# Kernel tuning notes

Hardware: AMD Instinct MI355X
Metric: run time of the kernel (lower is better)

Reference implementation:

```python
import jax, jax.numpy as jnp
import numpy as np
import math

HIDDEN = 2048
HEADS = 16
G = 4          # kv groups (= self.num_group after the module's head_num//num_group)
HPG = HEADS // G  # q heads per group
D = HIDDEN // HEADS  # 128


def setup_inputs() -> dict:
    key = jax.random.key(0)
    ks = jax.random.split(key, 9)
    B, S = 2, 2048
    s = 0.02
    return {
        "x": jax.random.normal(ks[0], (B, S, HIDDEN), dtype=jnp.float32),
        "Wq": jax.random.normal(ks[1], (HIDDEN, HIDDEN), dtype=jnp.float32) * s,
        "bq": jnp.zeros((HIDDEN,), jnp.float32),
        "Wk": jax.random.normal(ks[2], (HIDDEN, G * D), dtype=jnp.float32) * s,
        "bk": jnp.zeros((G * D,), jnp.float32),
        "Wv": jax.random.normal(ks[3], (HIDDEN, G * D), dtype=jnp.float32) * s,
        "bv": jnp.zeros((G * D,), jnp.float32),
        "Wo": jax.random.normal(ks[4], (HIDDEN, HIDDEN), dtype=jnp.float32) * s,
        "bo": jnpp if False else jnp.zeros((HIDDEN,), jnp.float32),
    }


def reference(x, Wq, bq, Wk, bk, Wv, bv, Wo, bo):
    B, S, H = x.shape
    # projections (torch Linear with W stored as (in, out))
    q = (x @ Wq + bq).reshape(B, S, G, HPG, D)   # (B,S,G,Hpg,D)
    k = (x @ Wk + bk).reshape(B, S, G, D)        # (B,S,G,D)
    v = (x @ Wv + bv).reshape(B, S, G, D)
    scale = 1.0 / math.sqrt(D)
    # scores: each of the Hpg query heads in a group shares the group's K/V
    scores = jnp.einsum("bsghd,btgd->bghst", q, k) * scale  # (B,G,Hpg,S,S)
    attn = jax.nn.softmax(scores, axis=-1)
    # dropout is identity in eval mode
    o = jnp.einsum("bghst,btgd->bsghd", attn, v).reshape(B, S, H)
    return o @ Wo + bo
```

## Files before the change

kernel.cpp:

```cpp
#include <hip/hip_runtime.h>

#define HID   2048
#define KD    2048
#define GQ    4
#define HPGQ  4
#define DH    128
#define SEQ   2048
#define NBATCH 2
#define NTOK  (NBATCH * SEQ)
#define NQKV  3072

typedef unsigned short u16;
typedef unsigned int   u32;
using bf16x8 = __attribute__((ext_vector_type(8))) __bf16;
using bf16x2 = __attribute__((ext_vector_type(2))) __bf16;
using f32x4  = __attribute__((ext_vector_type(4))) float;
using u32x4  = __attribute__((ext_vector_type(4))) u32;

#if __has_builtin(__builtin_amdgcn_exp2f)
#define FEXP2(x) __builtin_amdgcn_exp2f(x)
#else
#define FEXP2(x) exp2f(x)
#endif

#define QSCALE 0.12751744f

__device__ __forceinline__ u16 f2bf(float f) {
  union { float f; u32 u; } v; v.f = f;
  u32 u = v.u + 0x7fffu + ((v.u >> 16) & 1u);
  return (u16)(u >> 16);
}

__device__ __forceinline__ u32 pk2(float a, float b) {
  bf16x2 t;
  t[0] = (__bf16)a;
  t[1] = (__bf16)b;
  return __builtin_bit_cast(u32, t);
}

__device__ __forceinline__ void gl16(const void* g, void* l) {
  __builtin_amdgcn_global_load_lds((const __attribute__((address_space(1))) u32*)g,
                                   (__attribute__((address_space(3))) u32*)l, 16, 0, 0);
}

__device__ __forceinline__ int swz(int r, int c) {
  return (c & ~7) | ((c ^ r ^ (r >> 3)) & 7);
}

__global__ __launch_bounds__(256) void k_cvt_bf16(const float* __restrict__ in,
                                                  u16* __restrict__ out, int n4) {
  int i = blockIdx.x * 256 + threadIdx.x;
  if (i < n4) {
    const float4 v = ((const float4*)in)[i];
    ushort4 o;
    o.x = f2bf(v.x); o.y = f2bf(v.y); o.z = f2bf(v.z); o.w = f2bf(v.w);
    ((ushort4*)out)[i] = o;
  }
}

__global__ __launch_bounds__(256) void k_trans_cvt(const float* __restrict__ W,
                                                   u16* __restrict__ WT,
                                                   int K, int N, int rowoff) {
  __shared__ float tile[32][33];
  const int tx = threadIdx.x, ty = threadIdx.y;
  const int k0 = blockIdx.y * 32, n0 = blockIdx.x * 32;
#pragma unroll
  for (int i = 0; i < 4; ++i)
    tile[ty + 8 * i][tx] = W[(size_t)(k0 + ty + 8 * i) * N + (n0 + tx)];
  __syncthreads();
#pragma unroll
  for (int i = 0; i < 4; ++i)
    WT[(size_t)(rowoff + n0 + ty + 8 * i) * K + (k0 + tx)] = f2bf(tile[tx][ty + 8 * i]);
}


#define STG256(OP, ROWB, KTB, LB)                                                  \
  { _Pragma("unroll") for (int i = 0; i < 2; ++i)                                  \
      gl16((OP) + (size_t)(ROWB) * KD + (KTB) + stOffE[i],                         \
           S + (LB) + (i * 512 + t) * 8); }

#define STAGE_TILE(D, KTB)                                                         \
  STG256(A,  m0,       (KTB), (D) * 32768 + 0);                                    \
  STG256(A,  m0 + 128, (KTB), (D) * 32768 + 8192);                                 \
  STG256(Bt, n0,       (KTB), (D) * 32768 + 16384);                                \
  STG256(Bt, n0 + 128, (KTB), (D) * 32768 + 24576);

#define RDA(D, M, KC) (*(const bf16x8*)((const char*)S + (D) * 65536 + (M) * 2048 + (aQ ^ ((KC) << 6))))
#define RDB(D, N, KC) (*(const bf16x8*)((const char*)S + (D) * 65536 + (N) * 2048 + (bQ ^ ((KC) << 6))))

#define MFMA16(MB, NB)                                                             \
  __builtin_amdgcn_s_setprio(1);                                                   \
  _Pragma("unroll") for (int m = 0; m < 4; ++m)                                    \
    _Pragma("unroll") for (int n = 0; n < 2; ++n)                                  \
      _Pragma("unroll") for (int kc = 0; kc < 2; ++kc)                             \
        acc[(MB) + m][(NB) + n] = __builtin_amdgcn_mfma_f32_16x16x32_bf16(         \
            afr[m][kc], bfr[(NB) + n][kc], acc[(MB) + m][(NB) + n], 0, 0, 0);      \
  __builtin_amdgcn_s_setprio(0);

#define ITER256(D, KTN, PRE)                                                       \
  do {                                                                             \
                                     \
    _Pragma("unroll") for (int m = 0; m < 4; ++m)                                  \
      _Pragma("unroll") for (int kc = 0; kc < 2; ++kc)                             \
        afr[m][kc] = RDA(D, m, kc);                                                \
    _Pragma("unroll") for (int n = 0; n < 2; ++n)                                  \
      _Pragma("unroll") for (int kc = 0; kc < 2; ++kc)                             \
        bfr[n][kc] = RDB(D, n, kc);                                                \
    __builtin_amdgcn_s_barrier();                                                  \
    MFMA16(0, 0)                                                                   \
    __builtin_amdgcn_s_barrier();                                                  \
                                             \
    _Pragma("unroll") for (int n = 2; n < 4; ++n)                                  \
      _Pragma("unroll") for (int kc = 0; kc < 2; ++kc)                             \
        bfr[n][kc] = RDB(D, n, kc);                                                \
    __builtin_amdgcn_s_barrier();                                                  \
    MFMA16(0, 2)                                                                   \
    __builtin_amdgcn_s_barrier();                                                  \
                                 \
    _Pragma("unroll") for (int m = 0; m < 4; ++m)                                  \
      _Pragma("unroll") for (int kc = 0; kc < 2; ++kc)                             \
        afr[m][kc] = RDA(D, 4 + m, kc);                                            \
    __builtin_amdgcn_s_barrier();                                                  \
    MFMA16(4, 2)                                                                   \
    __builtin_amdgcn_s_barrier();                                                  \
             \
    if (PRE) {                                                                     \
      STAGE_TILE(D, KTN);                                                          \
      asm volatile("s_waitcnt vmcnt(8)" ::: "memory");                             \
    } else {                                                                       \
      asm volatile("s_waitcnt vmcnt(0)" ::: "memory");                             \
    }                                                                              \
    __builtin_amdgcn_s_barrier();                                                  \
    MFMA16(4, 0)                                                                   \
    __builtin_amdgcn_s_barrier();                                                  \
  } while (0)

__global__ __launch_bounds__(512, 1) void k_gemm_qkv(
    const u16* __restrict__ A, const u16* __restrict__ Bt,
    u16* __restrict__ qkv, u16* __restrict__ vT,
    const float* __restrict__ bq, const float* __restrict__ bk,
    const float* __restrict__ bv) {
  __shared__ u16 S[65536];
  const int t = threadIdx.x, l = t & 63, w = t >> 6;
  const int lr = l & 15, lk = l >> 4;
  const int wm = w >> 2, wn = w & 3;
  const int m0 = blockIdx.y * 256, n0 = blockIdx.x * 256;

  int stOffE[2];
#pragma unroll
  for (int i = 0; i < 2; ++i) {
    const int e = i * 512 + t;
    const int r = e >> 3;
    stOffE[i] = r * KD + ((e & 7) ^ (r & 7)) * 8;
  }
  const int qb = lr * 128 + (((lr >> 2) & 1) << 6) + ((lk ^ (lr & 3)) << 4);
  const int aQ = wm * 16384 + qb;
  const int bQ = 32768 + (wn >> 1) * 16384 + (wn & 1) * 8192 + qb;

  f32x4 acc[8][4] = {};
  bf16x8 afr[4][2], bfr[4][2];

  STAGE_TILE(0, 0);
  STAGE_TILE(1, 64);
  asm volatile("s_waitcnt vmcnt(8)" ::: "memory");
  __builtin_amdgcn_s_barrier();

  for (int j = 0; j < 28; j += 2) {
    ITER256(0, (j + 2) * 64, true);
    ITER256(1, (j + 3) * 64, true);
  }
  ITER256(0, 30 * 64, true);
  ITER256(1, 31 * 64, true);
  ITER256(0, 0, false);
  ITER256(1, 0, false);

  const int gmB = m0 + wm * 128, gnB = n0 + wn * 64;
#pragma unroll
  for (int m = 0; m < 8; ++m) {
    const int row0 = gmB + m * 16 + lk * 4;
#pragma unroll
    for (int n = 0; n < 4; ++n) {
      const int col = gnB + n * 16 + lr;
      float bias, qs = 1.0f;
      if (col < HID) { bias = bq[col]; qs = QSCALE; }
      else if (col < HID + 512) bias = bk[col - HID];
      else bias = bv[col - HID - 512];
      if (col < HID + 512) {
#pragma unroll
        for (int r = 0; r < 4; ++r)
          qkv[(size_t)(row0 + r) * NQKV + col] = f2bf((acc[m][n][r] + bias) * qs);
      } else {
        const int gg = (col - 2560) >> 7, d = (col - 2560) & 127;
        const int b = row0 >> 11, s0 = row0 & 2047;
        ushort4 pk;
        pk.x = f2bf(acc[m][n][0] + bias);
        pk.y = f2bf(acc[m][n][1] + bias);
        pk.z = f2bf(acc[m][n][2] + bias);
        pk.w = f2bf(acc[m][n][3] + bias);
        *(ushort4*)(vT + ((size_t)(b * GQ + gg) * DH + d) * SEQ + s0) = pk;
      }
    }
  }
}

#define GEMM_STEP(CUR, NXT, K0N, PRE)                                              \
  do {                                                                             \
    if (PRE) {                                                                     \
      const u16* aB = A  + (size_t)m0 * KD + (K0N);                                \
      const u16* bB = Bt + (size_t)n0 * KD + (K0N);                                \
      _Pragma("unroll")                                                            \
      for (int i = 0; i < 2; ++i) {                                                \
        gl16(aB + stOff[i], S + (NXT)*4096 + (i * 256 + t) * 8);                   \
        gl16(bB + stOff[i], S + 8192 + (NXT)*4096 + (i * 256 + t) * 8);            \
      }                                                                            \
      asm volatile("s_waitcnt vmcnt(4)" ::: "memory");                             \
    } else {                                                                       \
      asm volatile("s_waitcnt vmcnt(0)" ::: "memory");                             \
    }                                                                              \
    __builtin_amdgcn_s_barrier();                                                  \
    bf16x8 af[4], bfr[4];                                                          \
    _Pragma("unroll")                                                              \
    for (int m = 0; m < 4; ++m)                                                    \
      af[m] = *(const bf16x8*)((const char*)S + (CUR)*8192 + m * 1024 + aAddr);    \
    _Pragma("unroll")                                                              \
    for (int n = 0; n < 4; ++n)                                                    \
      bfr[n] = *(const bf16x8*)((const char*)S + 16384 + (CUR)*8192 + n * 1024 + bAddr); \
    __builtin_amdgcn_s_setprio(1);                                                 \
    _Pragma("unroll")                                                              \
    for (int m = 0; m < 4; ++m)                                                    \
      _Pragma("unroll")                                                            \
      for (int n = 0; n < 4; ++n)                                                  \
        acc[m][n] = __builtin_amdgcn_mfma_f32_16x16x32_bf16(af[m], bfr[n], acc[m][n], 0, 0, 0); \
    __builtin_amdgcn_s_setprio(0);                                                 \
    __builtin_amdgcn_s_barrier();                                                  \
  } while (0)

__global__ __launch_bounds__(256) void k_gemm_o(
    const u16* __restrict__ A, const u16* __restrict__ Bt,
    const float* __restrict__ bo, float* __restrict__ C) {
  __shared__ u16 S[16384];
  const int t = threadIdx.x, l = t & 63, w = t >> 6;
  const int lr = l & 15, lk = l >> 4;
  const int wr = w >> 1, wc = w & 1;
  const int m0 = blockIdx.y * 128, n0 = blockIdx.x * 128;
  int stOff[2];
#pragma unroll
  for (int i = 0; i < 2; ++i) {
    const int e = i * 256 + t;
    const int r = e >> 2;
    const int cs = (e & 3) ^ ((r >> 1) & 3);
    stOff[i] = r * KD + cs * 8;
  }
  const int axor = (lk ^ ((lr >> 1) & 3)) << 4;
  const int aAddr = (wr * 64 + lr) * 64 + axor;
  const int bAddr = (wc * 64 + lr) * 64 + axor;
  f32x4 acc[4][4] = {};
  {
    const u16* aB = A  + (size_t)m0 * KD;
    const u16* bB = Bt + (size_t)n0 * KD;
#pragma unroll
    for (int i = 0; i < 2; ++i) {
      gl16(aB + stOff[i], S + (i * 256 + t) * 8);
      gl16(bB + stOff[i], S + 8192 + (i * 256 + t) * 8);
    }
  }
  for (int kt = 0; kt < KD / 32 - 2; kt += 2) {
    GEMM_STEP(0, 1, (kt + 1) * 32, true);
    GEMM_STEP(1, 0, (kt + 2) * 32, true);
  }
  GEMM_STEP(0, 1, (KD / 32 - 1) * 32, true);
  GEMM_STEP(1, 0, 0, false);

  const int gm = m0 + wr * 64, gn = n0 + wc * 64;
#pragma unroll
  for (int m = 0; m < 4; ++m) {
    const int row0 = gm + m * 16 + lk * 4;
#pragma unroll
    for (int n = 0; n < 4; ++n) {
      const int col = gn + n * 16 + lr;
      const float bias = bo[col];
#pragma unroll
      for (int r = 0; r < 4; ++r)
        C[(size_t)(row0 + r) * HID + col] = acc[m][n][r] + bias;
    }
  }
}

#define ATTN_ITER(KS, VS, KN, VN, TTV, PRE)                                        \
  do {                                                                             \
    if (PRE) {                                                                     \
      const int t0n = ((start + (TTV) + 1) & (NT - 1)) * 32;                       \
      const u16* kbT = kbase + (size_t)t0n * NQKV;                                 \
      const u16* vbT = vbase + t0n;                                                \
      _Pragma("unroll")                                                            \
      for (int i = 0; i < 2; ++i) {                                                \
        gl16(kbT + kOffE[i], (KN) + (i * 256 + t) * 8);                            \
        gl16(vbT + vOffE[i], (VN) + (i * 256 + t) * 8);                            \
      }                                                                            \
      asm volatile("s_waitcnt vmcnt(4)" ::: "memory");                             \
    } else {                                                                       \
      asm volatile("s_waitcnt vmcnt(0)" ::: "memory");                             \
    }                                                                              \
    __builtin_amdgcn_s_barrier();                                                  \
    f32x4 sc[2][2] = {};                                                           \
    __builtin_amdgcn_s_setprio(1);                                                 \
    _Pragma("unroll")                                                              \
    for (int kk = 0; kk < 4; ++kk) {                                               \
      bf16x8 kf[2];                                                                \
      _Pragma("unroll")                                                            \
      for (int mk = 0; mk < 2; ++mk) {                                             \
        const int LIT = (mk << 12) ^ ((kk >> 1) << 7) ^ ((kk & 1) << 6) ^ (mk << 5); \
        kf[mk] = *(const bf16x8*)((const char*)(KS) + (kQ0 ^ LIT));                \
      }                                                                            \
      _Pragma("unroll")                                                            \
      for (int nq = 0; nq < 2; ++nq)                                               \
        _Pragma("unroll")                                                          \
        for (int mk = 0; mk < 2; ++mk)                                             \
          sc[nq][mk] = __builtin_amdgcn_mfma_f32_16x16x32_bf16(kf[mk], qf[nq][kk], sc[nq][mk], 0, 0, 0); \
    }                                                                              \
    __builtin_amdgcn_s_setprio(0);                                                 \
    bf16x8 pa[2];                                                                  \
    _Pragma("unroll")                                                              \
    for (int nq = 0; nq < 2; ++nq) {                                               \
      u32 w0 = pk2(FEXP2(sc[nq][0][0]), FEXP2(sc[nq][0][1]));                      \
      u32 w1 = pk2(FEXP2(sc[nq][0][2]), FEXP2(sc[nq][0][3]));                      \
      u32 w2 = pk2(FEXP2(sc[nq][1][0]), FEXP2(sc[nq][1][1]));                      \
      u32 w3 = pk2(FEXP2(sc[nq][1][2]), FEXP2(sc[nq][1][3]));                      \
      asm("v_permlane32_swap_b32 %0, %1" : "+v"(w0), "+v"(w2));                    \
      asm("v_permlane32_swap_b32 %0, %1" : "+v"(w1), "+v"(w3));                    \
      asm("v_permlane16_swap_b32 %0, %1" : "+v"(w0), "+v"(w2));                    \
      asm("v_permlane16_swap_b32 %0, %1" : "+v"(w1), "+v"(w3));                    \
      u32x4 u = {w0, w1, w2, w3};                                                  \
      pa[nq] = __builtin_bit_cast(bf16x8, u);                                      \
    }                                                                              \
    __builtin_amdgcn_s_setprio(1);                                                 \
    _Pragma("unroll")                                                              \
    for (int nq = 0; nq < 2; ++nq)                                                 \
      acc_s[nq] = __builtin_amdgcn_mfma_f32_16x16x32_bf16(pa[nq], vones, acc_s[nq], 0, 0, 0); \
    _Pragma("unroll")                                                              \
    for (int nd = 0; nd < 8; ++nd) {                                               \
      const bf16x8 vf = *(const bf16x8*)((const char*)(VS) + vQ0 + nd * 1024);     \
      _Pragma("unroll")                                                            \
      for (int nq = 0; nq < 2; ++nq)                                               \
        acc_o[nq][nd] = __builtin_amdgcn_mfma_f32_16x16x32_bf16(pa[nq], vf, acc_o[nq][nd], 0, 0, 0); \
    }                                                                              \
    __builtin_amdgcn_s_setprio(0);                                                 \
    __builtin_amdgcn_s_barrier();                                                  \
  } while (0)

__global__ __launch_bounds__(256, 2) void k_attn(
    const u16* __restrict__ qkv, const u16* __restrict__ vT, u16* __restrict__ o_ws) {
  __shared__ u16 smem[16384];
  u16* const kb0 = smem;
  u16* const kb1 = smem + 4096;
  u16* const vb0 = smem + 8192;
  u16* const vb1 = smem + 12288;

  const int t = threadIdx.x, l = t & 63, w = t >> 6;
  const int lr = l & 15, lk = l >> 4;
  const int f = blockIdx.x;
  const int bg = f & 7;
  const int h = (f >> 3) & 3;
  const int qt = f >> 5;
  const int b = bg >> 2, g = bg & 3;
  const int q0 = qt * 128;
  const int qcol = (g * HPGQ + h) * DH;
  const u16* qbase = qkv + (size_t)(b * SEQ) * NQKV;
  const u16* kbase = qbase + HID + g * DH;
  const u16* vbase = vT + (size_t)(b * GQ + g) * DH * SEQ;

  const int NT = SEQ / 32;
  const int start = (qt * 5 + h * 9) & (NT - 1);

  const int kQ0 = lr * 256 + ((lk ^ (lr & 7) ^ (lr >> 3)) << 4);
  const int vQ0 = lr * 64 + ((lk ^ ((lr >> 1) & 3)) << 4);
  int kOffE[2], vOffE[2];
#pragma unroll
  for (int i = 0; i < 2; ++i) {
    const int e = i * 256 + t;
    const int r = e >> 4, c = e & 15;
    kOffE[i] = r * NQKV + swz(r, c) * 8;
    const int rv = e >> 2, cv = e & 3;
    vOffE[i] = rv * SEQ + ((cv ^ ((rv >> 1) & 3)) * 8);
  }

  bf16x8 qf[2][4];
#pragma unroll
  for (int nq = 0; nq < 2; ++nq)
#pragma unroll
    for (int kk = 0; kk < 4; ++kk)
      qf[nq][kk] = *(const bf16x8*)(qbase + (size_t)(q0 + w * 32 + nq * 16 + lr) * NQKV +
                                    qcol + kk * 32 + lk * 8);

  {
    const int t00 = start * 32;
    const u16* kbT = kbase + (size_t)t00 * NQKV;
    const u16* vbT = vbase + t00;
#pragma unroll
    for (int i = 0; i < 2; ++i) {
      gl16(kbT + kOffE[i], kb0 + (i * 256 + t) * 8);
      gl16(vbT + vOffE[i], vb0 + (i * 256 + t) * 8);
    }
  }

  f32x4 acc_o[2][8] = {};
  f32x4 acc_s[2] = {};

  bf16x8 vones;
#pragma unroll
  for (int j = 0; j < 8; ++j) vones[j] = (lr == 0) ? (__bf16)1.0f : (__bf16)0.0f;

  for (int tp = 0; tp < NT - 2; tp += 2) {
    ATTN_ITER(kb0, vb0, kb1, vb1, tp, true);
    ATTN_ITER(kb1, vb1, kb0, vb0, tp + 1, true);
  }
  ATTN_ITER(kb0, vb0, kb1, vb1, NT - 2, true);
  ATTN_ITER(kb1, vb1, kb0, vb0, NT - 1, false);

#pragma unroll
  for (int nq = 0; nq < 2; ++nq)
#pragma unroll
    for (int r = 0; r < 4; ++r) {
      const float s = __shfl(acc_s[nq][r], l & 48);
      const float inv = 1.0f / s;
      const int q = q0 + w * 32 + nq * 16 + lk * 4 + r;
#pragma unroll
      for (int nd = 0; nd < 8; ++nd) {
        const int d = nd * 16 + lr;
        o_ws[(size_t)(b * SEQ + q) * HID + qcol + d] = f2bf(acc_o[nq][nd][r] * inv);
      }
    }
}

extern "C" void kernel_launch(void* const* d_in, const int* in_sizes, int n_in,
                              void* d_out, int out_size, void* d_ws, size_t ws_size,
                              hipStream_t stream) {
  const float* x  = (const float*)d_in[0];
  const float* Wq = (const float*)d_in[1];
  const float* bq = (const float*)d_in[2];
  const float* Wk = (const float*)d_in[3];
  const float* bk = (const float*)d_in[4];
  const float* Wv = (const float*)d_in[5];
  const float* bv = (const float*)d_in[6];
  const float* Wo = (const float*)d_in[7];
  const float* bo = (const float*)d_in[8];
  float* out = (float*)d_out;

  char* ws = (char*)d_ws;
  u16* x_bf  = (u16*)ws;  ws += (size_t)NTOK * KD * 2;
  u16* qkvT  = (u16*)ws;  ws += (size_t)NQKV * KD * 2;
  u16* WoT   = (u16*)ws;  ws += (size_t)HID * KD * 2;
  u16* qkv   = (u16*)ws;  ws += (size_t)NTOK * NQKV * 2;
  u16* vTb   = (u16*)ws;  ws += (size_t)NBATCH * GQ * DH * SEQ * 2;
  u16* o_ws  = x_bf;

  k_cvt_bf16<<<(NTOK * KD / 4 + 255) / 256, 256, 0, stream>>>(x, x_bf, NTOK * KD / 4);
  k_trans_cvt<<<dim3(HID / 32, KD / 32), dim3(32, 8), 0, stream>>>(Wq, qkvT, KD, HID, 0);
  k_trans_cvt<<<dim3(512 / 32, KD / 32), dim3(32, 8), 0, stream>>>(Wk, qkvT, KD, 512, 2048);
  k_trans_cvt<<<dim3(512 / 32, KD / 32), dim3(32, 8), 0, stream>>>(Wv, qkvT, KD, 512, 2560);
  k_trans_cvt<<<dim3(HID / 32, KD / 32), dim3(32, 8), 0, stream>>>(Wo, WoT, KD, HID, 0);

  k_gemm_qkv<<<dim3(NQKV / 256, NTOK / 256), 512, 0, stream>>>(x_bf, qkvT, qkv, vTb, bq, bk, bv);
  k_attn<<<SEQ / 128 * NBATCH * GQ * HPGQ, 256, 0, stream>>>(qkv, vTb, o_ws);
  k_gemm_o<<<dim3(HID / 128, NTOK / 128), 256, 0, stream>>>(o_ws, WoT, bo, out);
}
```

Before: 206.5 us.

## Retile QKV GEMM to 256x192 for full CU coverage and merge transpose launches

Changes the QKV projection GEMM tile from 256x256 to 256x192 so the grid has 256 blocks, matching the CU count and avoiding a partial second wave. It restructures LDS staging into separate A and B loads with adjusted waitcnts and a three-column-tile inner schedule. It also merges the four weight transpose/convert launches into one 3D-grid kernel to cut launch overhead. The smaller N tile lowers per-block arithmetic intensity and slightly increases A re-reads.

```diff
diff --git a/kernel.cpp b/kernel.cpp
--- a/kernel.cpp
+++ b/kernel.cpp
@@ -58,80 +58,101 @@
   }
 }
 
-__global__ __launch_bounds__(256) void k_trans_cvt(const float* __restrict__ W,
-                                                   u16* __restrict__ WT,
-                                                   int K, int N, int rowoff) {
+__global__ __launch_bounds__(256) void k_trans_all(
+    const float* __restrict__ Wq, const float* __restrict__ Wk,
+    const float* __restrict__ Wv, const float* __restrict__ Wo,
+    u16* __restrict__ qkvT, u16* __restrict__ WoT) {
   __shared__ float tile[32][33];
+  const int z = blockIdx.z;
+  const float* W = (z == 0) ? Wq : (z == 1) ? Wk : (z == 2) ? Wv : Wo;
+  u16* WT = (z == 3) ? WoT : qkvT;
+  const int N = (z == 1 || z == 2) ? 512 : 2048;
+  const int rowoff = (z == 1) ? 2048 : (z == 2) ? 2560 : 0;
+  const int n0 = blockIdx.x * 32;
+  if (n0 >= N) return;
   const int tx = threadIdx.x, ty = threadIdx.y;
-  const int k0 = blockIdx.y * 32, n0 = blockIdx.x * 32;
+  const int k0 = blockIdx.y * 32;
 #pragma unroll
   for (int i = 0; i < 4; ++i)
     tile[ty + 8 * i][tx] = W[(size_t)(k0 + ty + 8 * i) * N + (n0 + tx)];
   __syncthreads();
 #pragma unroll
   for (int i = 0; i < 4; ++i)
-    WT[(size_t)(rowoff + n0 + ty + 8 * i) * K + (k0 + tx)] = f2bf(tile[tx][ty + 8 * i]);
-}
-
-
-#define STG256(OP, ROWB, KTB, LB)                                                  \
+    WT[(size_t)(rowoff + n0 + ty + 8 * i) * KD + (k0 + tx)] = f2bf(tile[tx][ty + 8 * i]);
+}
+
+
+#define QBUF 114688
+#define BUFB 57344
+
+#define STG128(OP, ROWB, KTB, LBYTE)                                               \
   { _Pragma("unroll") for (int i = 0; i < 2; ++i)                                  \
       gl16((OP) + (size_t)(ROWB) * KD + (KTB) + stOffE[i],                         \
-           S + (LB) + (i * 512 + t) * 8); }
-
-#define STAGE_TILE(D, KTB)                                                         \
-  STG256(A,  m0,       (KTB), (D) * 32768 + 0);                                    \
-  STG256(A,  m0 + 128, (KTB), (D) * 32768 + 8192);                                 \
-  STG256(Bt, n0,       (KTB), (D) * 32768 + 16384);                                \
-  STG256(Bt, n0 + 128, (KTB), (D) * 32768 + 24576);
-
-#define RDA(D, M, KC) (*(const bf16x8*)((const char*)S + (D) * 65536 + (M) * 2048 + (aQ ^ ((KC) << 6))))
-#define RDB(D, N, KC) (*(const bf16x8*)((const char*)S + (D) * 65536 + (N) * 2048 + (bQ ^ ((KC) << 6))))
-
-#define MFMA16(MB, NB)                                                             \
-  __builtin_amdgcn_s_setprio(1);                                                   \
+           (u16*)((char*)S + (LBYTE)) + (i * 512 + t) * 8); }
+#define STG64(OP, ROWB, KTB, LBYTE)                                                \
+  gl16((OP) + (size_t)(ROWB) * KD + (KTB) + stOffE[0],                             \
+       (u16*)((char*)S + (LBYTE)) + t * 8);
+
+#define STAGE_B(D, KTB)                                                            \
+  STG128(Bt, n0b,       (KTB), (D) * BUFB + 32768);                                \
+  STG64 (Bt, n0b + 128, (KTB), (D) * BUFB + 49152);
+#define STAGE_A(D, KTB)                                                            \
+  STG128(A,  m0,        (KTB), (D) * BUFB + 0);                                    \
+  STG128(A,  m0 + 128,  (KTB), (D) * BUFB + 16384);
+
+#define RDA(D, M, KC) (*(const bf16x8*)((const char*)S + (D) * BUFB + (M) * 2048 + (aQ ^ ((KC) << 6))))
+#define RDB(D, NT, KC) (*(const bf16x8*)((const char*)S + (D) * BUFB + (NT) * 2048 + (bQ ^ ((KC) << 6))))
+
+#define MFMA8(MB, NT)                                                              \
   _Pragma("unroll") for (int m = 0; m < 4; ++m)                                    \
-    _Pragma("unroll") for (int n = 0; n < 2; ++n)                                  \
-      _Pragma("unroll") for (int kc = 0; kc < 2; ++kc)                             \
-        acc[(MB) + m][(NB) + n] = __builtin_amdgcn_mfma_f32_16x16x32_bf16(         \
-            afr[m][kc], bfr[(NB) + n][kc], acc[(MB) + m][(NB) + n], 0, 0, 0);      \
-  __builtin_amdgcn_s_setprio(0);
-
-#define ITER256(D, KTN, PRE)                                                       \
+    _Pragma("unroll") for (int kc = 0; kc < 2; ++kc)                               \
+      acc[(MB) + m][NT] = __builtin_amdgcn_mfma_f32_16x16x32_bf16(                 \
+          afr[m][kc], bfr[NT][kc], acc[(MB) + m][NT], 0, 0, 0);
+
+#define ITERQ(D, KTN, PRE)                                                         \
   do {                                                                             \
-                                     \
+                                                                           \
     _Pragma("unroll") for (int m = 0; m < 4; ++m)                                  \
       _Pragma("unroll") for (int kc = 0; kc < 2; ++kc)                             \
         afr[m][kc] = RDA(D, m, kc);                                                \
-    _Pragma("unroll") for (int n = 0; n < 2; ++n)                                  \
+    _Pragma("unroll") for (int nt = 0; nt < 2; ++nt)                               \
       _Pragma("unroll") for (int kc = 0; kc < 2; ++kc)                             \
-        bfr[n][kc] = RDB(D, n, kc);                                                \
-    __builtin_amdgcn_s_barrier();                                                  \
-    MFMA16(0, 0)                                                                   \
-    __builtin_amdgcn_s_barrier();                                                  \
-                                             \
-    _Pragma("unroll") for (int n = 2; n < 4; ++n)                                  \
-      _Pragma("unroll") for (int kc = 0; kc < 2; ++kc)                             \
-        bfr[n][kc] = RDB(D, n, kc);                                                \
-    __builtin_amdgcn_s_barrier();                                                  \
-    MFMA16(0, 2)                                                                   \
-    __builtin_amdgcn_s_barrier();                                                  \
-                                 \
+        bfr[nt][kc] = RDB(D, nt, kc);                                              \
+    asm volatile("s_waitcnt lgkmcnt(8)" ::: "memory");                             \
+    __builtin_amdgcn_s_barrier();                                                  \
+    __builtin_amdgcn_s_setprio(1);                                                 \
+    MFMA8(0, 0) MFMA8(0, 1)                                                        \
+    __builtin_amdgcn_s_setprio(0);                                                 \
+    __builtin_amdgcn_s_barrier();                                                  \
+                                                                           \
+    _Pragma("unroll") for (int kc = 0; kc < 2; ++kc)                               \
+      bfr[2][kc] = RDB(D, 2, kc);                                                  \
+    __builtin_amdgcn_s_barrier();                                                  \
+    __builtin_amdgcn_s_setprio(1);                                                 \
+    MFMA8(0, 2)                                                                    \
+    __builtin_amdgcn_s_setprio(0);                                                 \
+    __builtin_amdgcn_s_barrier();                                                  \
+                                                                           \
     _Pragma("unroll") for (int m = 0; m < 4; ++m)                                  \
       _Pragma("unroll") for (int kc = 0; kc < 2; ++kc)                             \
         afr[m][kc] = RDA(D, 4 + m, kc);                                            \
-    __builtin_amdgcn_s_barrier();                                                  \
-    MFMA16(4, 2)                                                                   \
-    __builtin_amdgcn_s_barrier();                                                  \
-             \
+    if (PRE) { STAGE_B(D, KTN); }                                                  \
+    __builtin_amdgcn_s_barrier();                                                  \
+    __builtin_amdgcn_s_setprio(1);                                                 \
+    MFMA8(4, 2)                                                                    \
+    __builtin_amdgcn_s_setprio(0);                                                 \
+    __builtin_amdgcn_s_barrier();                                                  \
+                                                                           \
     if (PRE) {                                                                     \
-      STAGE_TILE(D, KTN);                                                          \
-      asm volatile("s_waitcnt vmcnt(8)" ::: "memory");                             \
+      STAGE_A(D, KTN);                                                             \
+      asm volatile("s_waitcnt vmcnt(7)" ::: "memory");                             \
     } else {                                                                       \
       asm volatile("s_waitcnt vmcnt(0)" ::: "memory");                             \
     }                                                                              \
     __builtin_amdgcn_s_barrier();                                                  \
-    MFMA16(4, 0)                                                                   \
+    __builtin_amdgcn_s_setprio(1);                                                 \
+    MFMA8(4, 0) MFMA8(4, 1)                                                        \
+    __builtin_amdgcn_s_setprio(0);                                                 \
     __builtin_amdgcn_s_barrier();                                                  \
   } while (0)
 
@@ -140,11 +161,11 @@
     u16* __restrict__ qkv, u16* __restrict__ vT,
     const float* __restrict__ bq, const float* __restrict__ bk,
     const float* __restrict__ bv) {
-  __shared__ u16 S[65536];
+  __shared__ u16 S[QBUF / 2];
   const int t = threadIdx.x, l = t & 63, w = t >> 6;
   const int lr = l & 15, lk = l >> 4;
   const int wm = w >> 2, wn = w & 3;
-  const int m0 = blockIdx.y * 256, n0 = blockIdx.x * 256;
+  const int m0 = blockIdx.y * 256, n0b = blockIdx.x * 192;
 
   int stOffE[2];
 #pragma unroll
@@ -155,32 +176,30 @@
   }
   const int qb = lr * 128 + (((lr >> 2) & 1) << 6) + ((lk ^ (lr & 3)) << 4);
   const int aQ = wm * 16384 + qb;
-  const int bQ = 32768 + (wn >> 1) * 16384 + (wn & 1) * 8192 + qb;
-
-  f32x4 acc[8][4] = {};
-  bf16x8 afr[4][2], bfr[4][2];
-
-  STAGE_TILE(0, 0);
-  STAGE_TILE(1, 64);
-  asm volatile("s_waitcnt vmcnt(8)" ::: "memory");
+  const int bQ = 32768 + wn * 6144 + qb;
+
+  f32x4 acc[8][3] = {};
+  bf16x8 afr[4][2], bfr[3][2];
+
+  STAGE_A(0, 0);  STAGE_B(0, 0);
+  STAGE_A(1, 64); STAGE_B(1, 64);
+  asm volatile("s_waitcnt vmcnt(7)" ::: "memory");
   __builtin_amdgcn_s_barrier();
 
-  for (int j = 0; j < 28; j += 2) {
-    ITER256(0, (j + 2) * 64, true);
-    ITER256(1, (j + 3) * 64, true);
-  }
-  ITER256(0, 30 * 64, true);
-  ITER256(1, 31 * 64, true);
-  ITER256(0, 0, false);
-  ITER256(1, 0, false);
-
-  const int gmB = m0 + wm * 128, gnB = n0 + wn * 64;
+  for (int j = 0; j < 30; j += 2) {
+    ITERQ(0, (j + 2) * 64, true);
+    ITERQ(1, (j + 3) * 64, true);
+  }
+  ITERQ(0, 0, false);
+  ITERQ(1, 0, false);
+
+  const int gmB = m0 + wm * 128, gnB = n0b + wn * 48;
 #pragma unroll
   for (int m = 0; m < 8; ++m) {
     const int row0 = gmB + m * 16 + lk * 4;
 #pragma unroll
-    for (int n = 0; n < 4; ++n) {
-      const int col = gnB + n * 16 + lr;
+    for (int nt = 0; nt < 3; ++nt) {
+      const int col = gnB + nt * 16 + lr;
       float bias, qs = 1.0f;
       if (col < HID) { bias = bq[col]; qs = QSCALE; }
       else if (col < HID + 512) bias = bk[col - HID];
@@ -188,15 +207,15 @@
       if (col < HID + 512) {
 #pragma unroll
         for (int r = 0; r < 4; ++r)
-          qkv[(size_t)(row0 + r) * NQKV + col] = f2bf((acc[m][n][r] + bias) * qs);
+          qkv[(size_t)(row0 + r) * NQKV + col] = f2bf((acc[m][nt][r] + bias) * qs);
       } else {
         const int gg = (col - 2560) >> 7, d = (col - 2560) & 127;
         const int b = row0 >> 11, s0 = row0 & 2047;
         ushort4 pk;
-        pk.x = f2bf(acc[m][n][0] + bias);
-        pk.y = f2bf(acc[m][n][1] + bias);
-        pk.z = f2bf(acc[m][n][2] + bias);
-        pk.w = f2bf(acc[m][n][3] + bias);
+        pk.x = f2bf(acc[m][nt][0] + bias);
+        pk.y = f2bf(acc[m][nt][1] + bias);
+        pk.z = f2bf(acc[m][nt][2] + bias);
+        pk.w = f2bf(acc[m][nt][3] + bias);
         *(ushort4*)(vT + ((size_t)(b * GQ + gg) * DH + d) * SEQ + s0) = pk;
       }
     }
@@ -210,8 +229,8 @@
       const u16* bB = Bt + (size_t)n0 * KD + (K0N);                                \
       _Pragma("unroll")                                                            \
       for (int i = 0; i < 2; ++i) {                                                \
-        gl16(aB + stOff[i], S + (NXT)*4096 + (i * 256 + t) * 8);                   \
-        gl16(bB + stOff[i], S + 8192 + (NXT)*4096 + (i * 256 + t) * 8);            \
+        gl16(aB + stOff[i], So + (NXT)*4096 + (i * 256 + t) * 8);                  \
+        gl16(bB + stOff[i], So + 8192 + (NXT)*4096 + (i * 256 + t) * 8);           \
       }                                                                            \
       asm volatile("s_waitcnt vmcnt(4)" ::: "memory");                             \
     } else {                                                                       \
@@ -221,10 +240,10 @@
     bf16x8 af[4], bfr[4];                                                          \
     _Pragma("unroll")                                                              \
     for (int m = 0; m < 4; ++m)                                                    \
-      af[m] = *(const bf16x8*)((const char*)S + (CUR)*8192 + m * 1024 + aAddr);    \
+      af[m] = *(const bf16x8*)((const char*)So + (CUR)*8192 + m * 1024 + aAddr);   \
     _Pragma("unroll")                                                              \
     for (int n = 0; n < 4; ++n)                                                    \
-      bfr[n] = *(const bf16x8*)((const char*)S + 16384 + (CUR)*8192 + n * 1024 + bAddr); \
+      bfr[n] = *(const bf16x8*)((const char*)So + 16384 + (CUR)*8192 + n * 1024 + bAddr); \
     __builtin_amdgcn_s_setprio(1);                                                 \
     _Pragma("unroll")                                                              \
     for (int m = 0; m < 4; ++m)                                                    \
@@ -238,7 +257,7 @@
 __global__ __launch_bounds__(256) void k_gemm_o(
     const u16* __restrict__ A, const u16* __restrict__ Bt,
     const float* __restrict__ bo, float* __restrict__ C) {
-  __shared__ u16 S[16384];
+  __shared__ u16 So[16384];
   const int t = threadIdx.x, l = t & 63, w = t >> 6;
   const int lr = l & 15, lk = l >> 4;
   const int wr = w >> 1, wc = w & 1;
@@ -260,8 +279,8 @@
     const u16* bB = Bt + (size_t)n0 * KD;
 #pragma unroll
     for (int i = 0; i < 2; ++i) {
-      gl16(aB + stOff[i], S + (i * 256 + t) * 8);
-      gl16(bB + stOff[i], S + 8192 + (i * 256 + t) * 8);
+      gl16(aB + stOff[i], So + (i * 256 + t) * 8);
+      gl16(bB + stOff[i], So + 8192 + (i * 256 + t) * 8);
     }
   }
   for (int kt = 0; kt < KD / 32 - 2; kt += 2) {
@@ -455,12 +474,9 @@
   u16* o_ws  = x_bf;
 
   k_cvt_bf16<<<(NTOK * KD / 4 + 255) / 256, 256, 0, stream>>>(x, x_bf, NTOK * KD / 4);
-  k_trans_cvt<<<dim3(HID / 32, KD / 32), dim3(32, 8), 0, stream>>>(Wq, qkvT, KD, HID, 0);
-  k_trans_cvt<<<dim3(512 / 32, KD / 32), dim3(32, 8), 0, stream>>>(Wk, qkvT, KD, 512, 2048);
-  k_trans_cvt<<<dim3(512 / 32, KD / 32), dim3(32, 8), 0, stream>>>(Wv, qkvT, KD, 512, 2560);
-  k_trans_cvt<<<dim3(HID / 32, KD / 32), dim3(32, 8), 0, stream>>>(Wo, WoT, KD, HID, 0);
-
-  k_gemm_qkv<<<dim3(NQKV / 256, NTOK / 256), 512, 0, stream>>>(x_bf, qkvT, qkv, vTb, bq, bk, bv);
+  k_trans_all<<<dim3(64, 64, 4), dim3(32, 8), 0, stream>>>(Wq, Wk, Wv, Wo, qkvT, WoT);
+
+  k_gemm_qkv<<<dim3(NQKV / 192, NTOK / 256), 512, 0, stream>>>(x_bf, qkvT, qkv, vTb, bq, bk, bv);
   k_attn<<<SEQ / 128 * NBATCH * GQ * HPGQ, 256, 0, stream>>>(qkv, vTb, o_ws);
   k_gemm_o<<<dim3(HID / 128, NTOK / 128), 256, 0, stream>>>(o_ws, WoT, bo, out);
 }
```

New measurement: 186.9 us. 9.4% less time.
